# Optimization experiments

Hardware: AMD Instinct MI355X
Metric: run time of the kernel (lower is better)

Reference implementation:

```python
import jax, jax.numpy as jnp
import numpy as np

B, DIN, HID, COMP = 16384, 1024, 512, 64

def setup_inputs() -> dict:
    key = jax.random.key(0)
    ks = jax.random.split(key, 16)
    s = lambda fan_in: 1.0 / np.sqrt(fan_in)
    return {
        "x1": jax.random.normal(ks[0], (B, DIN), jnp.float32),
        "x2": jax.random.normal(ks[1], (B, DIN), jnp.float32),
        "Wb1": jax.random.normal(ks[2], (DIN, HID), jnp.float32) * s(DIN),
        "bb1": jnp.zeros((HID,), jnp.float32),
        "Wb2": jax.random.normal(ks[3], (DIN, HID), jnp.float32) * s(DIN),
        "bb2": jnp.zeros((HID,), jnp.float32),
        "Wc1": jax.random.normal(ks[4], (HID, COMP), jnp.float32) * s(HID),
        "bc1": jnp.zeros((COMP,), jnp.float32),
        "Wc2": jax.random.normal(ks[5], (HID, COMP), jnp.float32) * s(HID),
        "bc2": jnp.zeros((COMP,), jnp.float32),
        "Wf1": jax.random.normal(ks[6], (COMP * COMP, 64), jnp.float32) * s(COMP * COMP),
        "bf1": jnp.zeros((64,), jnp.float32),
        "Wf2": jax.random.normal(ks[7], (64, 2), jnp.float32) * s(64),
        "bf2": jnp.zeros((2,), jnp.float32),
    }

def reference(x1, x2, Wb1, bb1, Wb2, bb2, Wc1, bc1, Wc2, bc2, Wf1, bf1, Wf2, bf2):
    # branch + compress: [B, DIN] -> [B, HID] -> [B, COMP]
    f1 = (jax.nn.relu(x1 @ Wb1 + bb1)) @ Wc1 + bc1  # [B, 64]
    f2 = (jax.nn.relu(x2 @ Wb2 + bb2)) @ Wc2 + bc2  # [B, 64]
    # kronecker_product(f1, f2): per-sample (f2 col) * (f1 row) -> [64,64], row-major flatten
    # element at flat index p*64 + q is f2[p] * f1[q]
    kron = jnp.einsum('bp,bq->bpq', f2, f1).reshape(f1.shape[0], -1)  # [B, 4096]
    h = kron @ Wf1 + bf1   # [B, 64]
    out = h @ Wf2 + bf2    # [B, 2]
    return out
```

## Files before the change

### kernel.cpp

```cpp
#include <hip/hip_runtime.h>

#define B_SZ 16384
#define DIN  1024
#define HID  512
#define COMP 64

typedef __bf16 bf16_t;
typedef __bf16 bf16x4 __attribute__((ext_vector_type(4)));
typedef __bf16 bf16x8 __attribute__((ext_vector_type(8)));
typedef float  f32x4  __attribute__((ext_vector_type(4)));

#define MFMA16 __builtin_amdgcn_mfma_f32_16x16x32_bf16

__device__ __forceinline__ void gl2lds16(const void* g, void* l) {
    __builtin_amdgcn_global_load_lds(
        (const __attribute__((address_space(1))) void*)g,
        (__attribute__((address_space(3))) void*)l, 16, 0, 0);
}

__global__ __launch_bounds__(256) void k_prep(
    const float* __restrict__ Wb1, const float* __restrict__ Wb2,
    bf16_t* __restrict__ wbt1, bf16_t* __restrict__ wbt2,
    const float* __restrict__ Wc1, const float* __restrict__ Wc2,
    bf16_t* __restrict__ wct1, bf16_t* __restrict__ wct2,
    const float* __restrict__ Wf1, const float* __restrict__ bf1v,
    const float* __restrict__ Wf2, const float* __restrict__ bf2v,
    const float* __restrict__ bc1, const float* __restrict__ bc2,
    float* __restrict__ f1, float* __restrict__ f2,
    const float* __restrict__ x1, const float* __restrict__ x2,
    bf16_t* __restrict__ xb1, bf16_t* __restrict__ xb2,
    float* __restrict__ G, float* __restrict__ c)
{
    const int bid = blockIdx.x, tid = threadIdx.x;

    if (bid >= 3152) {
        const int l = bid - 3152;
        const int z = l >> 13;
        const float* x  = z ? x2  : x1;
        bf16_t*      xb = z ? xb2 : xb1;
        const size_t base = ((size_t)(l & 8191) * 256 + tid) * 8;
        float4 v0 = *reinterpret_cast<const float4*>(x + base);
        float4 v1 = *reinterpret_cast<const float4*>(x + base + 4);
        bf16x8 o;
        o[0] = (bf16_t)v0.x; o[1] = (bf16_t)v0.y;
        o[2] = (bf16_t)v0.z; o[3] = (bf16_t)v0.w;
        o[4] = (bf16_t)v1.x; o[5] = (bf16_t)v1.y;
        o[6] = (bf16_t)v1.z; o[7] = (bf16_t)v1.w;
        *reinterpret_cast<bf16x8*>(xb + base) = o;
        return;
    }

    __shared__ float tile[32][33];
    const int tx = tid & 31, ty = tid >> 5;

    if (bid < 1024) {
        const int z = bid >> 9, t = bid & 511;
        const float* in  = z ? Wb2  : Wb1;
        bf16_t*      out = z ? wbt2 : wbt1;
        const int n0 = (t & 15) * 32, k0 = (t >> 4) * 32;
        #pragma unroll
        for (int i = 0; i < 4; i++)
            tile[ty + i * 8][tx] = in[(size_t)(k0 + ty + i * 8) * HID + n0 + tx];
        __syncthreads();
        #pragma unroll
        for (int i = 0; i < 4; i++)
            out[(size_t)(n0 + ty + i * 8) * DIN + k0 + tx] = (bf16_t)tile[tx][ty + i * 8];
    } else if (bid < 1088) {
        const int l = bid - 1024;
        const int z = l >> 5, t = l & 31;
        const float* in  = z ? Wc2  : Wc1;
        bf16_t*      out = z ? wct2 : wct1;
        const int n0 = (t & 1) * 32, k0 = (t >> 1) * 32;
        #pragma unroll
        for (int i = 0; i < 4; i++)
            tile[ty + i * 8][tx] = in[(size_t)(k0 + ty + i * 8) * COMP + n0 + tx];
        __syncthreads();
        #pragma unroll
        for (int i = 0; i < 4; i++)
            out[(size_t)(n0 + ty + i * 8) * HID + k0 + tx] = (bf16_t)tile[tx][ty + i * 8];
    } else if (bid < 1104) {
        const int i = (bid - 1088) * 256 + tid;
        float a0 = 0.f, a1 = 0.f;
        #pragma unroll 8
        for (int o = 0; o < 64; o++) {
            float w = Wf1[(size_t)i * 64 + o];
            a0 = fmaf(w, Wf2[o * 2 + 0], a0);
            a1 = fmaf(w, Wf2[o * 2 + 1], a1);
        }
        G[i]        = a0;
        G[4096 + i] = a1;
        if (i < 2) {
            float s = bf2v[i];
            for (int o = 0; o < 64; o++) s = fmaf(bf1v[o], Wf2[o * 2 + i], s);
            c[i] = s;
        }
    } else {
        const int l = bid - 1104;
        const int z = l >> 10;
        const float* bc = z ? bc2 : bc1;
        float*       f  = z ? f2  : f1;
        const int i = (l & 1023) * 256 + tid;
        const int c4 = (i & 15) * 4;
        float4 v = make_float4(bc[c4], bc[c4 + 1], bc[c4 + 2], bc[c4 + 3]);
        reinterpret_cast<float4*>(f)[i] = v;
    }
}

__global__ __launch_bounds__(512, 2) void k_gemm1f(
    const bf16_t* __restrict__ XB1, const bf16_t* __restrict__ XB2,
    const bf16_t* __restrict__ WT1, const bf16_t* __restrict__ WT2,
    const float* __restrict__ bias1, const float* __restrict__ bias2,
    const bf16_t* __restrict__ WC1, const bf16_t* __restrict__ WC2,
    float* __restrict__ F1, float* __restrict__ F2)
{
    const int bid = blockIdx.x;
    const int nid = (bid & 7) * 32 + (bid >> 3);
    const int z   = nid >> 7;
    const int nb  = (nid >> 6) & 1;
    const int mb  = nid & 63;

    const bf16_t* XB   = z ? XB2   : XB1;
    const bf16_t* WT   = z ? WT2   : WT1;
    const float*  bias = z ? bias2 : bias1;
    const bf16_t* WC   = z ? WC2   : WC1;
    float*        F    = z ? F2    : F1;

    const int m0 = mb * 256;
    const int n0 = nb * 256;

    __shared__ __align__(128) char smem[135168];

    const int tid  = threadIdx.x;
    const int lane = tid & 63;
    const int wave = tid >> 6;
    const int wm   = wave >> 2;
    const int wn   = wave & 3;
    const int l15  = lane & 15;
    const int g4   = lane >> 4;

    const int srow = tid >> 3;
    const int sch  = (tid & 7) ^ (srow & 7);
    const bf16_t* gA = XB + (size_t)(m0 + srow) * DIN + sch * 8;
    const bf16_t* gB = WT + (size_t)(n0 + srow) * DIN + sch * 8;
    const int ldst = tid * 16;

    const int l7   = l15 & 7;
    const int lch0 = (g4 ^ l7) * 16;
    const int lch1 = ((4 + g4) ^ l7) * 16;
    const int abase = (wm * 64 + l15) * 128;
    const int bbase = (wn * 64 + l15) * 128;

    f32x4 acc[2][4][4] = {};

    gl2lds16(gA,                        smem + ldst);
    gl2lds16(gA + (size_t)64 * DIN,     smem + 8192 + ldst);
    gl2lds16(gA + (size_t)128 * DIN,    smem + 16384 + ldst);
    gl2lds16(gA + (size_t)192 * DIN,    smem + 24576 + ldst);
    gl2lds16(gB,                        smem + 65536 + ldst);
    gl2lds16(gB + (size_t)64 * DIN,     smem + 65536 + 8192 + ldst);
    gl2lds16(gB + (size_t)128 * DIN,    smem + 65536 + 16384 + ldst);
    gl2lds16(gB + (size_t)192 * DIN,    smem + 65536 + 24576 + ldst);
    gl2lds16(gA + 64,                   smem + 32768 + ldst);
    gl2lds16(gA + 64 + (size_t)64 * DIN, smem + 32768 + 8192 + ldst);
    __builtin_amdgcn_sched_barrier(0);

    #pragma unroll 1
    for (int kt = 0; kt < 16; ++kt) {
        const int d = kt & 1;
        const char* Ac = smem + d * 32768;
        const char* Bc = smem + 65536 + d * 32768;
        char* An = (char*)smem + (d ^ 1) * 32768;
        char* Bn = (char*)smem + 65536 + (d ^ 1) * 32768;
        char* An2 = (char*)smem + d * 32768;
        const bf16_t* gA1 = gA + (kt + 1) * 64;
        const bf16_t* gA2 = gA + (kt + 2) * 64;
        const bf16_t* gB1 = gB + (kt + 1) * 64;

        gl2lds16(gA1 + (size_t)128 * DIN, An + 16384 + ldst);
        gl2lds16(gA1 + (size_t)192 * DIN, An + 24576 + ldst);
        gl2lds16(gB1,                     Bn + ldst);
        gl2lds16(gB1 + (size_t)64 * DIN,  Bn + 8192 + ldst);
        gl2lds16(gB1 + (size_t)128 * DIN, Bn + 16384 + ldst);
        gl2lds16(gB1 + (size_t)192 * DIN, Bn + 24576 + ldst);
        __builtin_amdgcn_sched_barrier(0);
        asm volatile("s_waitcnt vmcnt(8)" ::: "memory");
        __builtin_amdgcn_s_barrier();
        __builtin_amdgcn_sched_barrier(0);

        bf16x8 a[4][2], b[4][2];
        #pragma unroll
        for (int mi = 0; mi < 4; mi++) {
            a[mi][0] = *(const bf16x8*)(Ac + abase + mi * 2048 + lch0);
            a[mi][1] = *(const bf16x8*)(Ac + abase + mi * 2048 + lch1);
        }
        #pragma unroll
        for (int ni = 0; ni < 4; ni++) {
            b[ni][0] = *(const bf16x8*)(Bc + bbase + ni * 2048 + lch0);
            b[ni][1] = *(const bf16x8*)(Bc + bbase + ni * 2048 + lch1);
        }
        __builtin_amdgcn_s_setprio(1);
        #pragma unroll
        for (int mi = 0; mi < 4; mi++)
            #pragma unroll
            for (int ni = 0; ni < 4; ni++) {
                acc[0][mi][ni] = MFMA16(a[mi][0], b[ni][0], acc[0][mi][ni], 0, 0, 0);
                acc[0][mi][ni] = MFMA16(a[mi][1], b[ni][1], acc[0][mi][ni], 0, 0, 0);
            }
        __builtin_amdgcn_s_setprio(0);
        __builtin_amdgcn_sched_barrier(0);
        __builtin_amdgcn_s_barrier();
        __builtin_amdgcn_sched_barrier(0);

        gl2lds16(gA2,                     An2 + ldst);
        gl2lds16(gA2 + (size_t)64 * DIN,  An2 + 8192 + ldst);
        __builtin_amdgcn_sched_barrier(0);

        bf16x8 a2[4][2];
        #pragma unroll
        for (int mi = 0; mi < 4; mi++) {
            a2[mi][0] = *(const bf16x8*)(Ac + 16384 + abase + mi * 2048 + lch0);
            a2[mi][1] = *(const bf16x8*)(Ac + 16384 + abase + mi * 2048 + lch1);
        }
        __builtin_amdgcn_s_setprio(1);
        #pragma unroll
        for (int mi = 0; mi < 4; mi++)
            #pragma unroll
            for (int ni = 0; ni < 4; ni++) {
                acc[1][mi][ni] = MFMA16(a2[mi][0], b[ni][0], acc[1][mi][ni], 0, 0, 0);
                acc[1][mi][ni] = MFMA16(a2[mi][1], b[ni][1], acc[1][mi][ni], 0, 0, 0);
            }
        __builtin_amdgcn_s_setprio(0);
        __builtin_amdgcn_sched_barrier(0);
        __builtin_amdgcn_s_barrier();
        __builtin_amdgcn_sched_barrier(0);
    }

    asm volatile("s_waitcnt vmcnt(0)" ::: "memory");
    __builtin_amdgcn_s_barrier();

    bf16_t* Hs = (bf16_t*)smem;
    float bv[4];
    #pragma unroll
    for (int ni = 0; ni < 4; ni++)
        bv[ni] = bias[n0 + wn * 64 + ni * 16 + l15];
    #pragma unroll
    for (int ph = 0; ph < 2; ph++) {
        #pragma unroll
        for (int mi = 0; mi < 4; mi++) {
            const int lr = ph * 128 + wm * 64 + mi * 16 + g4 * 4;
            #pragma unroll
            for (int ni = 0; ni < 4; ni++) {
                const int colL = wn * 64 + ni * 16 + l15;
                #pragma unroll
                for (int r = 0; r < 4; r++) {
                    float v = fmaxf(acc[ph][mi][ni][r] + bv[ni], 0.0f);
                    Hs[(lr + r) * 264 + colL] = (bf16_t)v;
                }
            }
        }
    }
    __syncthreads();

    f32x4 acc2[2][4] = {};
    #pragma unroll
    for (int kk = 0; kk < 256; kk += 32) {
        bf16x8 af2[2];
        #pragma unroll
        for (int m2 = 0; m2 < 2; m2++)
            af2[m2] = *(const bf16x8*)(Hs + (wave * 32 + m2 * 16 + l15) * 264 + kk + g4 * 8);
        #pragma unroll
        for (int ni = 0; ni < 4; ni++) {
            bf16x8 bw = *(const bf16x8*)(&WC[(size_t)(ni * 16 + l15) * HID + n0 + kk + g4 * 8]);
            #pragma unroll
            for (int m2 = 0; m2 < 2; m2++)
                acc2[m2][ni] = MFMA16(af2[m2], bw, acc2[m2][ni], 0, 0, 0);
        }
    }
    #pragma unroll
    for (int m2 = 0; m2 < 2; m2++) {
        const int rbase = m0 + wave * 32 + m2 * 16 + g4 * 4;
        #pragma unroll
        for (int ni = 0; ni < 4; ni++) {
            const int col = ni * 16 + l15;
            #pragma unroll
            for (int r = 0; r < 4; r++)
                unsafeAtomicAdd(&F[(size_t)(rbase + r) * COMP + col], acc2[m2][ni][r]);
        }
    }
}

__global__ __launch_bounds__(256) void k_bilinear(
    const float* __restrict__ f1, const float* __restrict__ f2,
    const float* __restrict__ G, const float* __restrict__ c,
    float* __restrict__ out)
{
    __shared__ float Gs[2][4096];
    const int tid = threadIdx.x;
    for (int i = tid; i < 2048; i += 256)
        reinterpret_cast<float4*>(&Gs[0][0])[i] =
            reinterpret_cast<const float4*>(G)[i];
    const float c0 = c[0], c1 = c[1];
    __syncthreads();

    const int lane = tid & 63;
    const int wave = tid >> 6;
    const int base = (blockIdx.x * 4 + wave) * 4;

    for (int s = 0; s < 4; s++) {
        const int b = base + s;
        const float f1q = f1[(size_t)b * 64 + lane];
        const float f2q = f2[(size_t)b * 64 + lane];
        float a0 = 0.f, a1 = 0.f;
        #pragma unroll 8
        for (int p = 0; p < 64; p++) {
            float s2 = __shfl(f2q, p);
            a0 = fmaf(s2, Gs[0][p * 64 + lane], a0);
            a1 = fmaf(s2, Gs[1][p * 64 + lane], a1);
        }
        a0 *= f1q;
        a1 *= f1q;
        #pragma unroll
        for (int off = 32; off > 0; off >>= 1) {
            a0 += __shfl_xor(a0, off);
            a1 += __shfl_xor(a1, off);
        }
        if (lane == 0) {
            out[(size_t)b * 2 + 0] = a0 + c0;
            out[(size_t)b * 2 + 1] = a1 + c1;
        }
    }
}

extern "C" void kernel_launch(void* const* d_in, const int* in_sizes, int n_in,
                              void* d_out, int out_size, void* d_ws, size_t ws_size,
                              hipStream_t stream)
{
    const float* x1  = (const float*)d_in[0];
    const float* x2  = (const float*)d_in[1];
    const float* Wb1 = (const float*)d_in[2];
    const float* bb1 = (const float*)d_in[3];
    const float* Wb2 = (const float*)d_in[4];
    const float* bb2 = (const float*)d_in[5];
    const float* Wc1 = (const float*)d_in[6];
    const float* bc1 = (const float*)d_in[7];
    const float* Wc2 = (const float*)d_in[8];
    const float* bc2 = (const float*)d_in[9];
    const float* Wf1 = (const float*)d_in[10];
    const float* bf1v = (const float*)d_in[11];
    const float* Wf2 = (const float*)d_in[12];
    const float* bf2v = (const float*)d_in[13];
    float* out = (float*)d_out;

    char* ws = (char*)d_ws;
    bf16_t* wbt1 = (bf16_t*)ws; ws += (size_t)HID * DIN * 2;
    bf16_t* wbt2 = (bf16_t*)ws; ws += (size_t)HID * DIN * 2;
    bf16_t* wct1 = (bf16_t*)ws; ws += (size_t)COMP * HID * 2;
    bf16_t* wct2 = (bf16_t*)ws; ws += (size_t)COMP * HID * 2;
    bf16_t* xb1  = (bf16_t*)ws; ws += (size_t)B_SZ * DIN * 2;
    bf16_t* xb2  = (bf16_t*)ws; ws += (size_t)B_SZ * DIN * 2;
    float*  f1   = (float*)ws;  ws += (size_t)B_SZ * COMP * 4;
    float*  f2   = (float*)ws;  ws += (size_t)B_SZ * COMP * 4;
    float*  G    = (float*)ws;  ws += (size_t)2 * 4096 * 4;
    float*  c    = (float*)ws;  ws += 256;

    k_prep<<<19536, 256, 0, stream>>>(Wb1, Wb2, wbt1, wbt2,
                                      Wc1, Wc2, wct1, wct2,
                                      Wf1, bf1v, Wf2, bf2v,
                                      bc1, bc2, f1, f2,
                                      x1, x2, xb1, xb2, G, c);
    k_gemm1f<<<256, 512, 0, stream>>>(xb1, xb2, wbt1, wbt2, bb1, bb2,
                                      wct1, wct2, f1, f2);
    k_bilinear<<<1024, 256, 0, stream>>>(f1, f2, G, c, out);
}
```

Before: 246.0 us.

## Register-block bilinear over 64-sample tiles and coarsen fp32-to-bf16 conversion

The bilinear kernel now stages each block's 64 samples of f1 and f2 transposed in LDS. Each lane owns one sample and accumulates 32 partial outputs in registers, reading G as broadcast float4 loads instead of using per-element shuffles. A final LDS reduction combines the two q-halves. Separately, the input conversion path has each thread handle 8 chunks across x1 and x2, which cuts the prep launch from 19536 to 5200 blocks. The bilinear grid drops to 256 blocks with about 67KB of LDS each, which may limit occupancy and latency hiding.

```diff
diff --git a/kernel.cpp b/kernel.cpp
--- a/kernel.cpp
+++ b/kernel.cpp
@@ -34,19 +34,23 @@
     const int bid = blockIdx.x, tid = threadIdx.x;
 
     if (bid >= 3152) {
-        const int l = bid - 3152;
-        const int z = l >> 13;
-        const float* x  = z ? x2  : x1;
-        bf16_t*      xb = z ? xb2 : xb1;
-        const size_t base = ((size_t)(l & 8191) * 256 + tid) * 8;
-        float4 v0 = *reinterpret_cast<const float4*>(x + base);
-        float4 v1 = *reinterpret_cast<const float4*>(x + base + 4);
-        bf16x8 o;
-        o[0] = (bf16_t)v0.x; o[1] = (bf16_t)v0.y;
-        o[2] = (bf16_t)v0.z; o[3] = (bf16_t)v0.w;
-        o[4] = (bf16_t)v1.x; o[5] = (bf16_t)v1.y;
-        o[6] = (bf16_t)v1.z; o[7] = (bf16_t)v1.w;
-        *reinterpret_cast<bf16x8*>(xb + base) = o;
+        const int i0 = (bid - 3152) * 256 + tid;
+        #pragma unroll
+        for (int k = 0; k < 8; k++) {
+            const float* x  = (k < 4) ? x1  : x2;
+            bf16_t*      xb = (k < 4) ? xb2 : xb2;
+            xb = (k < 4) ? xb1 : xb2;
+            const size_t ch = (size_t)i0 + (size_t)(k & 3) * 524288;
+            const size_t base = ch * 8;
+            float4 v0 = *reinterpret_cast<const float4*>(x + base);
+            float4 v1 = *reinterpret_cast<const float4*>(x + base + 4);
+            bf16x8 o;
+            o[0] = (bf16_t)v0.x; o[1] = (bf16_t)v0.y;
+            o[2] = (bf16_t)v0.z; o[3] = (bf16_t)v0.w;
+            o[4] = (bf16_t)v1.x; o[5] = (bf16_t)v1.y;
+            o[6] = (bf16_t)v1.z; o[7] = (bf16_t)v1.w;
+            *reinterpret_cast<bf16x8*>(xb + base) = o;
+        }
         return;
     }
 
@@ -295,39 +299,64 @@
     float* __restrict__ out)
 {
     __shared__ float Gs[2][4096];
+    __shared__ float f1t[64][66];
+    __shared__ float f2t[64][66];
+    __shared__ float part[4][64];
+
     const int tid = threadIdx.x;
+    const int s0  = blockIdx.x * 64;
+
     for (int i = tid; i < 2048; i += 256)
         reinterpret_cast<float4*>(&Gs[0][0])[i] =
             reinterpret_cast<const float4*>(G)[i];
-    const float c0 = c[0], c1 = c[1];
+
+    #pragma unroll
+    for (int rr = 0; rr < 4; rr++) {
+        const int row = (tid >> 4) + rr * 16;
+        const int c4  = (tid & 15) * 4;
+        float4 v1 = *reinterpret_cast<const float4*>(&f1[(size_t)(s0 + row) * 64 + c4]);
+        float4 v2 = *reinterpret_cast<const float4*>(&f2[(size_t)(s0 + row) * 64 + c4]);
+        f1t[c4 + 0][row] = v1.x; f1t[c4 + 1][row] = v1.y;
+        f1t[c4 + 2][row] = v1.z; f1t[c4 + 3][row] = v1.w;
+        f2t[c4 + 0][row] = v2.x; f2t[c4 + 1][row] = v2.y;
+        f2t[c4 + 2][row] = v2.z; f2t[c4 + 3][row] = v2.w;
+    }
     __syncthreads();
 
     const int lane = tid & 63;
-    const int wave = tid >> 6;
-    const int base = (blockIdx.x * 4 + wave) * 4;
-
-    for (int s = 0; s < 4; s++) {
-        const int b = base + s;
-        const float f1q = f1[(size_t)b * 64 + lane];
-        const float f2q = f2[(size_t)b * 64 + lane];
-        float a0 = 0.f, a1 = 0.f;
-        #pragma unroll 8
-        for (int p = 0; p < 64; p++) {
-            float s2 = __shfl(f2q, p);
-            a0 = fmaf(s2, Gs[0][p * 64 + lane], a0);
-            a1 = fmaf(s2, Gs[1][p * 64 + lane], a1);
-        }
-        a0 *= f1q;
-        a1 *= f1q;
-        #pragma unroll
-        for (int off = 32; off > 0; off >>= 1) {
-            a0 += __shfl_xor(a0, off);
-            a1 += __shfl_xor(a1, off);
-        }
-        if (lane == 0) {
-            out[(size_t)b * 2 + 0] = a0 + c0;
-            out[(size_t)b * 2 + 1] = a1 + c1;
-        }
+    const int wv   = tid >> 6;
+    const int j    = wv & 1;
+    const int qh   = (wv >> 1) * 32;
+
+    float tq[32];
+    #pragma unroll
+    for (int q = 0; q < 32; q++) tq[q] = 0.f;
+
+    #pragma unroll 4
+    for (int p = 0; p < 64; p++) {
+        const float f2p = f2t[p][lane];
+        const float* Gp = &Gs[j][p * 64 + qh];
+        #pragma unroll
+        for (int q4 = 0; q4 < 8; q4++) {
+            float4 g = *reinterpret_cast<const float4*>(Gp + q4 * 4);
+            tq[q4 * 4 + 0] = fmaf(f2p, g.x, tq[q4 * 4 + 0]);
+            tq[q4 * 4 + 1] = fmaf(f2p, g.y, tq[q4 * 4 + 1]);
+            tq[q4 * 4 + 2] = fmaf(f2p, g.z, tq[q4 * 4 + 2]);
+            tq[q4 * 4 + 3] = fmaf(f2p, g.w, tq[q4 * 4 + 3]);
+        }
+    }
+
+    float o = 0.f;
+    #pragma unroll
+    for (int q = 0; q < 32; q++)
+        o = fmaf(f1t[qh + q][lane], tq[q], o);
+
+    part[wv][lane] = o;
+    __syncthreads();
+
+    if (wv < 2) {
+        float r = part[wv][lane] + part[wv + 2][lane] + c[wv];
+        out[(size_t)(s0 + lane) * 2 + wv] = r;
     }
 }
 
@@ -363,12 +392,12 @@
     float*  G    = (float*)ws;  ws += (size_t)2 * 4096 * 4;
     float*  c    = (float*)ws;  ws += 256;
 
-    k_prep<<<19536, 256, 0, stream>>>(Wb1, Wb2, wbt1, wbt2,
-                                      Wc1, Wc2, wct1, wct2,
-                                      Wf1, bf1v, Wf2, bf2v,
-                                      bc1, bc2, f1, f2,
-                                      x1, x2, xb1, xb2, G, c);
+    k_prep<<<5200, 256, 0, stream>>>(Wb1, Wb2, wbt1, wbt2,
+                                     Wc1, Wc2, wct1, wct2,
+                                     Wf1, bf1v, Wf2, bf2v,
+                                     bc1, bc2, f1, f2,
+                                     x1, x2, xb1, xb2, G, c);
     k_gemm1f<<<256, 512, 0, stream>>>(xb1, xb2, wbt1, wbt2, bb1, bb2,
                                       wct1, wct2, f1, f2);
-    k_bilinear<<<1024, 256, 0, stream>>>(f1, f2, G, c, out);
+    k_bilinear<<<256, 256, 0, stream>>>(f1, f2, G, c, out);
 }
```

Result: no change. 243.7 us (-0.9%).
